# Kernel optimization log

Measured on AMD Instinct MI355X. Metric: run time of the kernel, lower is better.

Reference implementation:

```python
import jax, jax.numpy as jnp
import numpy as np

L = 6      # layers (enc and dec)
D = 512    # d_model
H = 8      # heads
DK = D // H
F = 2048   # dim_feedforward
B = 8
S = 512    # src len
T = 512    # tgt len
NEG = -1e9


def setup_inputs() -> dict:
    key = jax.random.key(0)
    ks = jax.random.split(key, 64)
    it = iter(ks)
    def w(shape, scale=0.02):
        return jax.random.normal(next(it), shape, dtype=jnp.float32) * scale
    inp = {}
    inp['src'] = jax.random.normal(next(it), (B, S, D), dtype=jnp.float32)
    inp['tgt'] = jax.random.normal(next(it), (B, T, D), dtype=jnp.float32)
    inp['tgt_mask'] = jnp.where(jnp.triu(jnp.ones((T, T), bool), 1), jnp.float32(NEG), jnp.float32(0.0))
    # encoder params (stacked over L layers)
    inp['enc_Wq'] = w((L, H, D, DK)); inp['enc_Wk'] = w((L, H, D, DK)); inp['enc_Wv'] = w((L, H, D, DK))
    inp['enc_Wo'] = w((L, D, D))
    inp['enc_ln1_a'] = jnp.ones((L, D)); inp['enc_ln1_b'] = jnp.zeros((L, D))
    inp['enc_W1'] = w((L, D, F)); inp['enc_b1'] = jnp.zeros((L, F))
    inp['enc_W2'] = w((L, F, D)); inp['enc_b2'] = jnp.zeros((L, D))
    inp['enc_ln2_a'] = jnp.ones((L, D)); inp['enc_ln2_b'] = jnp.zeros((L, D))
    # decoder params
    inp['dec_sWq'] = w((L, H, D, DK)); inp['dec_sWk'] = w((L, H, D, DK)); inp['dec_sWv'] = w((L, H, D, DK))
    inp['dec_sWo'] = w((L, D, D))
    inp['dec_ln1_a'] = jnp.ones((L, D)); inp['dec_ln1_b'] = jnp.zeros((L, D))
    inp['dec_cWq'] = w((L, H, D, DK)); inp['dec_cWk'] = w((L, H, D, DK)); inp['dec_cWv'] = w((L, H, D, DK))
    inp['dec_cWo'] = w((L, D, D))
    inp['dec_ln2_a'] = jnp.ones((L, D)); inp['dec_ln2_b'] = jnp.zeros((L, D))
    inp['dec_W1'] = w((L, D, F)); inp['dec_b1'] = jnp.zeros((L, F))
    inp['dec_W2'] = w((L, F, D)); inp['dec_b2'] = jnp.zeros((L, D))
    inp['dec_ln3_a'] = jnp.ones((L, D)); inp['dec_ln3_b'] = jnp.zeros((L, D))
    return inp


def layernorm(x, a, b):
    # faithful to the torch module: unbiased std (ddof=1) and eps added to std
    mean = x.mean(-1, keepdims=True)
    std = jnp.std(x, axis=-1, keepdims=True, ddof=1)
    return a * (x - mean) / (std + 1e-6) + b


def mha(qx, kx, vx, Wq, Wk, Wv, Wo, mask):
    # Wq/Wk/Wv: [H, D, dk] (per-head torch loop fused into one batched einsum)
    q = jnp.einsum('bsd,hdk->bhsk', qx, Wq)
    k = jnp.einsum('bsd,hdk->bhsk', kx, Wk)
    v = jnp.einsum('bsd,hdk->bhsk', vx, Wv)
    scores = jnp.einsum('bhqk,bhmk->bhqm', q, k) / np.float32(np.sqrt(Wq.shape[-1]))
    if mask is not None:
        scores = scores + mask  # [T,T] broadcasts over batch and heads
    attn = jax.nn.softmax(scores, axis=-1)
    o = jnp.einsum('bhqm,bhmk->bhqk', attn, v)
    b_, h_, s_, k_ = o.shape
    o = o.transpose(0, 2, 1, 3).reshape(b_, s_, h_ * k_)  # concat heads
    return o @ Wo


def ffn(x, W1, b1, W2, b2):
    return jnp.maximum(x @ W1 + b1, 0.0) @ W2 + b2


def reference(src, tgt, tgt_mask,
              enc_Wq, enc_Wk, enc_Wv, enc_Wo, enc_ln1_a, enc_ln1_b,
              enc_W1, enc_b1, enc_W2, enc_b2, enc_ln2_a, enc_ln2_b,
              dec_sWq, dec_sWk, dec_sWv, dec_sWo, dec_ln1_a, dec_ln1_b,
              dec_cWq, dec_cWk, dec_cWv, dec_cWo, dec_ln2_a, dec_ln2_b,
              dec_W1, dec_b1, dec_W2, dec_b2, dec_ln3_a, dec_ln3_b):
    # encoder
    x = src
    for i in range(L):
        h = x + mha(x, x, x, enc_Wq[i], enc_Wk[i], enc_Wv[i], enc_Wo[i], None)
        x = layernorm(h, enc_ln1_a[i], enc_ln1_b[i])
        h = x + ffn(x, enc_W1[i], enc_b1[i], enc_W2[i], enc_b2[i])
        x = layernorm(h, enc_ln2_a[i], enc_ln2_b[i])
    memory = x
    # decoder
    y = tgt
    for i in range(L):
        h = y + mha(y, y, y, dec_sWq[i], dec_sWk[i], dec_sWv[i], dec_sWo[i], tgt_mask)
        y = layernorm(h, dec_ln1_a[i], dec_ln1_b[i])
        h = y + mha(y, memory, memory, dec_cWq[i], dec_cWk[i], dec_cWv[i], dec_cWo[i], None)
        y = layernorm(h, dec_ln2_a[i], dec_ln2_b[i])
        h = y + ffn(y, dec_W1[i], dec_b1[i], dec_W2[i], dec_b2[i])
        y = layernorm(h, dec_ln3_a[i], dec_ln3_b[i])
    return y
```

## Files before the change

kernel.cpp:

```cpp
#include <hip/hip_runtime.h>
#include <hip/hip_bf16.h>

typedef unsigned short u16;
typedef __hip_bfloat16 hbf;
typedef __bf16 bf16x8 __attribute__((ext_vector_type(8)));
typedef float f32x4 __attribute__((ext_vector_type(4)));

#define LL 6
#define DD 512
#define HH 8
#define DKK 64
#define FF 2048
#define BB 8
#define SS 512

__global__ __launch_bounds__(256) void cvt_k(const float* __restrict__ x,
                                             hbf* __restrict__ y, int n) {
  for (int i = (blockIdx.x * 256 + threadIdx.x) * 4; i < n; i += gridDim.x * 1024) {
    float4 v = *(const float4*)(x + i);
    y[i] = __float2bfloat16(v.x);
    y[i + 1] = __float2bfloat16(v.y);
    y[i + 2] = __float2bfloat16(v.z);
    y[i + 3] = __float2bfloat16(v.w);
  }
}

__global__ __launch_bounds__(256) void transpose_k(const float* __restrict__ src,
                                                   hbf* __restrict__ dst, int R, int C) {
  __shared__ hbf tile[64][65];
  const int b = blockIdx.z;
  src += (size_t)b * R * C;
  dst += (size_t)b * R * C;
  int c0 = blockIdx.x * 64, r0 = blockIdx.y * 64;
  int tx = threadIdx.x & 63;
  int ty = threadIdx.x >> 6;
#pragma unroll
  for (int i = 0; i < 16; i++) {
    int r = ty + i * 4;
    tile[r][tx] = __float2bfloat16(src[(size_t)(r0 + r) * C + c0 + tx]);
  }
  __syncthreads();
#pragma unroll
  for (int i = 0; i < 16; i++) {
    int r = ty + i * 4;
    dst[(size_t)(c0 + r) * R + r0 + tx] = tile[tx][r];
  }
}

__global__ __launch_bounds__(256) void transpose_qkv_k(const float* __restrict__ Wq,
                                                       const float* __restrict__ Wk,
                                                       const float* __restrict__ Wv,
                                                       hbf* __restrict__ dst) {
  __shared__ hbf tile[64][65];
  const int z = blockIdx.z;
  const int l = z / 24, r = z - l * 24;
  const int zw = r >> 3, h = r & 7;
  const float* src =
      (zw == 0 ? Wq : (zw == 1 ? Wk : Wv)) + ((size_t)l * HH + h) * DD * DKK;
  const int r0 = blockIdx.y * 64;
  const int tx = threadIdx.x & 63, ty = threadIdx.x >> 6;
#pragma unroll
  for (int i = 0; i < 16; i++) {
    int rr = ty + i * 4;
    tile[rr][tx] = __float2bfloat16(src[(size_t)(r0 + rr) * DKK + tx]);
  }
  __syncthreads();
  hbf* d = dst + (size_t)l * 3 * DD * DD + ((size_t)zw * 512 + h * 64) * DD + r0;
#pragma unroll
  for (int i = 0; i < 16; i++) {
    int rr = ty + i * 4;
    d[(size_t)rr * DD + tx] = tile[tx][rr];
  }
}

template <int BM, int BN, int BK, int MODE, int SPLITK>
__global__ __launch_bounds__(256) void gemm_nt(
    const u16* __restrict__ A, const u16* __restrict__ Bm, void* __restrict__ Cout,
    void* __restrict__ C2, void* __restrict__ C3,
    const float* __restrict__ bias, const hbf* __restrict__ res,
    int M, int N, int K, int lda, int ldb, int ldc, int ncoloff,
    long sAo, long sAi, long sBo, long sBi, long sCo, long sCi, int inner, float scale) {
  constexpr int WVM = (BM == 128 && BN == 128) ? 2 : (BM == 128 ? 4 : 2);
  constexpr int WVN = 4 / WVM;
  constexpr int WTM = BM / WVM, WTN = BN / WVN;
  constexpr int AM = WTM / 16, AN = WTN / 16;
  constexpr int PA = (BM * BK) / 2048, PB = (BN * BK) / 2048;
  constexpr int CPR = BK / 8;
  __shared__ u16 As[BM][BK + 8];
  __shared__ u16 Bs[BN][BK + 8];

  int g = blockIdx.z;
  int ks = 0;
  if (SPLITK > 1) {
    ks = g;
    g = 0;
  }
  int outer = g / inner, inr = g - outer * inner;
  A += outer * sAo + inr * sAi;
  Bm += outer * sBo + inr * sBi;

  const int tid = threadIdx.x;
  const int m0 = blockIdx.y * BM, n0 = (blockIdx.x + ncoloff) * BN;
  const int wave = tid >> 6, lane = tid & 63;
  const int wm = (wave / WVN) * WTM, wn = (wave % WVN) * WTN;
  const int m16 = lane & 15, quad = lane >> 4;

  const u16* Ab = A + (size_t)m0 * lda;
  const u16* Bb = Bm + (size_t)n0 * ldb;

  f32x4 acc[AM][AN] = {};

  const int kbeg = ks * (K / SPLITK), kend = kbeg + K / SPLITK;
  for (int k0 = kbeg; k0 < kend; k0 += BK) {
#pragma unroll
    for (int p = 0; p < PA; p++) {
      int idx = p * 256 + tid;
      int row = idx / CPR, ch = (idx % CPR) * 8;
      *(float4*)(&As[row][ch]) = *(const float4*)(Ab + (size_t)row * lda + k0 + ch);
    }
#pragma unroll
    for (int p = 0; p < PB; p++) {
      int idx = p * 256 + tid;
      int row = idx / CPR, ch = (idx % CPR) * 8;
      *(float4*)(&Bs[row][ch]) = *(const float4*)(Bb + (size_t)row * ldb + k0 + ch);
    }
    __syncthreads();
#pragma unroll
    for (int kc = 0; kc < BK / 32; kc++) {
      bf16x8 af[AM], bfv[AN];
#pragma unroll
      for (int i = 0; i < AM; i++)
        af[i] = *(const bf16x8*)(&As[wm + i * 16 + m16][kc * 32 + quad * 8]);
#pragma unroll
      for (int j = 0; j < AN; j++)
        bfv[j] = *(const bf16x8*)(&Bs[wn + j * 16 + m16][kc * 32 + quad * 8]);
#pragma unroll
      for (int i = 0; i < AM; i++)
#pragma unroll
        for (int j = 0; j < AN; j++)
          acc[i][j] = __builtin_amdgcn_mfma_f32_16x16x32_bf16(af[i], bfv[j], acc[i][j], 0, 0, 0);
    }
    __syncthreads();
  }

#pragma unroll
  for (int i = 0; i < AM; i++) {
#pragma unroll
    for (int j = 0; j < AN; j++) {
      const int col = n0 + wn + j * 16 + m16;
      const int rowb = m0 + wm + i * 16 + quad * 4;
#pragma unroll
      for (int r = 0; r < 4; r++) {
        const int row = rowb + r;
        float v = acc[i][j][r] * scale;
        if (MODE == 0) {
          hbf* C = (hbf*)Cout + outer * sCo + inr * sCi;
          C[(size_t)row * ldc + col] = __float2bfloat16(v);
        } else if (MODE == 2) {
          float* C = (float*)((SPLITK > 1 && ks == 1) ? C2 : Cout);
          C += outer * sCo + inr * sCi;
          if (SPLITK == 1 || ks == 0) {
            if (bias) v += bias[col];
            if (res) v += __bfloat162float(res[(size_t)row * ldc + col]);
          }
          C[(size_t)row * ldc + col] = v;
        } else if (MODE == 3) {
          hbf* C = (hbf*)Cout + outer * sCo + inr * sCi;
          v += bias[col];
          C[(size_t)row * ldc + col] = __float2bfloat16(fmaxf(v, 0.0f));
        } else if (MODE == 4) {
          const int b = row >> 9, s = row & 511;
          const int which = col >> 9, h = (col >> 6) & 7, dk = col & 63;
          const int bh = (b << 3) + h;
          if (which == 0)
            ((hbf*)Cout)[((size_t)bh * SS + s) * DKK + dk] = __float2bfloat16(v * 0.125f);
          else if (which == 1)
            ((hbf*)C2)[((size_t)bh * SS + s) * DKK + dk] = __float2bfloat16(v);
          else
            ((hbf*)C3)[((size_t)bh * DKK + dk) * SS + s] = __float2bfloat16(v);
        }
      }
    }
  }
}

__global__ __launch_bounds__(256) void softmax_k(hbf* __restrict__ P, int causal) {
  const int row = blockIdx.x;
  hbf* p = P + ((size_t)blockIdx.y * SS + row) * SS;
  const int t = threadIdx.x;
  const int c0 = 2 * t, c1 = 2 * t + 1;
  float v0 = __bfloat162float(p[c0]);
  float v1 = __bfloat162float(p[c1]);
  if (causal) {
    if (c0 > row) v0 = -1e30f;
    if (c1 > row) v1 = -1e30f;
  }
  float m = fmaxf(v0, v1);
#pragma unroll
  for (int off = 32; off > 0; off >>= 1) m = fmaxf(m, __shfl_down(m, off));
  __shared__ float sm[4];
  __shared__ float bc;
  const int wv = t >> 6, ln = t & 63;
  if (ln == 0) sm[wv] = m;
  __syncthreads();
  if (t == 0) bc = fmaxf(fmaxf(sm[0], sm[1]), fmaxf(sm[2], sm[3]));
  __syncthreads();
  m = bc;
  float e0 = __expf(v0 - m), e1 = __expf(v1 - m);
  float s = e0 + e1;
#pragma unroll
  for (int off = 32; off > 0; off >>= 1) s += __shfl_down(s, off);
  __syncthreads();
  if (ln == 0) sm[wv] = s;
  __syncthreads();
  if (t == 0) bc = sm[0] + sm[1] + sm[2] + sm[3];
  __syncthreads();
  const float inv = 1.0f / bc;
  p[c0] = __float2bfloat16(e0 * inv);
  p[c1] = __float2bfloat16(e1 * inv);
}

template <typename T>
__global__ __launch_bounds__(256) void layernorm_k(const float* __restrict__ X,
                                                   const float* __restrict__ X2,
                                                   const float* __restrict__ ga,
                                                   const float* __restrict__ gb,
                                                   T* __restrict__ out, int Dn) {
  const int row = blockIdx.x;
  X += (size_t)row * Dn;
  X2 += (size_t)row * Dn;
  out += (size_t)row * Dn;
  const int t = threadIdx.x;
  float2 xv = *(const float2*)(X + 2 * t);
  float2 x2 = *(const float2*)(X2 + 2 * t);
  xv.x += x2.x;
  xv.y += x2.y;
  float s = xv.x + xv.y, ss = xv.x * xv.x + xv.y * xv.y;
#pragma unroll
  for (int off = 32; off > 0; off >>= 1) {
    s += __shfl_down(s, off);
    ss += __shfl_down(ss, off);
  }
  __shared__ float sm[8];
  __shared__ float smean, sinv;
  const int wv = t >> 6, ln = t & 63;
  if (ln == 0) {
    sm[wv] = s;
    sm[4 + wv] = ss;
  }
  __syncthreads();
  if (t == 0) {
    float S1 = sm[0] + sm[1] + sm[2] + sm[3];
    float S2 = sm[4] + sm[5] + sm[6] + sm[7];
    float mean = S1 / Dn;
    float var = (S2 - S1 * mean) / (Dn - 1);
    var = fmaxf(var, 0.0f);
    smean = mean;
    sinv = 1.0f / (sqrtf(var) + 1e-6f);
  }
  __syncthreads();
  const float mean = smean, inv = sinv;
  float o0 = ga[2 * t] * (xv.x - mean) * inv + gb[2 * t];
  float o1 = ga[2 * t + 1] * (xv.y - mean) * inv + gb[2 * t + 1];
  if constexpr (sizeof(T) == 2) {
    out[2 * t] = (T)__float2bfloat16(o0);
    out[2 * t + 1] = (T)__float2bfloat16(o1);
  } else {
    out[2 * t] = o0;
    out[2 * t + 1] = o1;
  }
}

extern "C" void kernel_launch(void* const* d_in, const int* in_sizes, int n_in,
                              void* d_out, int out_size, void* d_ws, size_t ws_size,
                              hipStream_t stream) {
  (void)in_sizes; (void)n_in; (void)out_size;
  const float* src = (const float*)d_in[0];
  const float* tgt = (const float*)d_in[1];
  const float* eWq = (const float*)d_in[3];
  const float* eWk = (const float*)d_in[4];
  const float* eWv = (const float*)d_in[5];
  const float* eWo = (const float*)d_in[6];
  const float* eln1a = (const float*)d_in[7];
  const float* eln1b = (const float*)d_in[8];
  const float* eW1 = (const float*)d_in[9];
  const float* eb1 = (const float*)d_in[10];
  const float* eW2 = (const float*)d_in[11];
  const float* eb2 = (const float*)d_in[12];
  const float* eln2a = (const float*)d_in[13];
  const float* eln2b = (const float*)d_in[14];
  const float* sWq = (const float*)d_in[15];
  const float* sWk = (const float*)d_in[16];
  const float* sWv = (const float*)d_in[17];
  const float* sWo = (const float*)d_in[18];
  const float* dln1a = (const float*)d_in[19];
  const float* dln1b = (const float*)d_in[20];
  const float* cWq = (const float*)d_in[21];
  const float* cWk = (const float*)d_in[22];
  const float* cWv = (const float*)d_in[23];
  const float* cWo = (const float*)d_in[24];
  const float* dln2a = (const float*)d_in[25];
  const float* dln2b = (const float*)d_in[26];
  const float* dW1 = (const float*)d_in[27];
  const float* db1 = (const float*)d_in[28];
  const float* dW2 = (const float*)d_in[29];
  const float* db2 = (const float*)d_in[30];
  const float* dln3a = (const float*)d_in[31];
  const float* dln3b = (const float*)d_in[32];

  const size_t MB = 1024 * 1024;
  char* ws = (char*)d_ws;
  const size_t QKV_L = (size_t)3 * DD * DD;
  const size_t WO_L = (size_t)DD * DD;
  const size_t WF_L = (size_t)DD * FF;
  const bool preT = ws_size >= 145 * MB;

  hbf *qkvT_all = nullptr, *woT_all = nullptr, *w1T_all = nullptr, *w2T_all = nullptr;
  hbf *wqkvS = nullptr, *woS = nullptr, *w1S = nullptr, *w2S = nullptr;
  char* actb;
  if (preT) {
    qkvT_all = (hbf*)(ws);
    woT_all = (hbf*)(ws + 28311552);
    w1T_all = (hbf*)(ws + 37748736);
    w2T_all = (hbf*)(ws + 62914560);
    actb = ws + 84 * MB;
  } else {
    if (ws_size < 67 * MB) return;
    wqkvS = (hbf*)(ws);
    woS = (hbf*)(ws + 2 * MB);
    w1S = (hbf*)(ws + 2 * MB + 512 * 1024);
    w2S = (hbf*)(ws + 4 * MB + 512 * 1024);
    actb = ws + 7 * MB;
  }
  hbf* sbuf = (hbf*)(actb);
  u16* xbuf = (u16*)(actb + 4 * MB);
  hbf* tbuf = (hbf*)(actb + 8 * MB);
  u16* ybuf = (u16*)(actb + 12 * MB);
  u16* qbuf = (u16*)(actb + 16 * MB);
  u16* kbuf = (u16*)(actb + 20 * MB);
  u16* vtb = (u16*)(actb + 24 * MB);
  u16* attnb = (u16*)(actb + 28 * MB);
  float* projf = (float*)(actb + 28 * MB);
  u16* ffnh = (u16*)(actb + 36 * MB);
  float* projf2 = (float*)(actb + 52 * MB);

  const long SD = (long)SS * DD;
  const long SDK = (long)SS * DKK;
  const long DKS = (long)DKK * SS;
  const long SSq = (long)SS * SS;
  const size_t WQL = (size_t)HH * DD * DKK;
  const size_t WOL = (size_t)DD * DD;
  const size_t WFL = (size_t)DD * FF;

  if (preT) {
    transpose_qkv_k<<<dim3(1, 8, LL * 24), dim3(256), 0, stream>>>(eWq, eWk, eWv, qkvT_all);
    transpose_qkv_k<<<dim3(1, 8, LL * 24), dim3(256), 0, stream>>>(sWq, sWk, sWv,
                                                                   qkvT_all + LL * QKV_L);
    transpose_qkv_k<<<dim3(1, 8, LL * 24), dim3(256), 0, stream>>>(
        cWq, cWk, cWv, qkvT_all + 2 * LL * QKV_L);
    transpose_k<<<dim3(8, 8, LL), dim3(256), 0, stream>>>(eWo, woT_all, DD, DD);
    transpose_k<<<dim3(8, 8, LL), dim3(256), 0, stream>>>(sWo, woT_all + LL * WO_L, DD, DD);
    transpose_k<<<dim3(8, 8, LL), dim3(256), 0, stream>>>(cWo, woT_all + 2 * LL * WO_L, DD, DD);
    transpose_k<<<dim3(32, 8, LL), dim3(256), 0, stream>>>(eW1, w1T_all, DD, FF);
    transpose_k<<<dim3(32, 8, LL), dim3(256), 0, stream>>>(dW1, w1T_all + LL * WF_L, DD, FF);
    transpose_k<<<dim3(8, 32, LL), dim3(256), 0, stream>>>(eW2, w2T_all, FF, DD);
    transpose_k<<<dim3(8, 32, LL), dim3(256), 0, stream>>>(dW2, w2T_all + LL * WF_L, FF, DD);
  }

  auto attention = [&](const u16* qin, const u16* kvin, const hbf* qkvTl, const hbf* woTl,
                       const u16* resid, int causal) {
    if (qin == kvin) {
      gemm_nt<64, 64, 128, 4, 1><<<dim3(24, 64, 1), dim3(256), 0, stream>>>(
          qin, (const u16*)qkvTl, qbuf, kbuf, vtb, nullptr, nullptr, BB * SS, 3 * DD, DD,
          DD, DD, 0, 0, 0, 0, 0, 0, 0, 0, 1, 1.f);
    } else {
      gemm_nt<64, 64, 128, 4, 1><<<dim3(8, 64, 1), dim3(256), 0, stream>>>(
          qin, (const u16*)qkvTl, qbuf, kbuf, vtb, nullptr, nullptr, BB * SS, DD, DD,
          DD, DD, 0, 0, 0, 0, 0, 0, 0, 0, 1, 1.f);
      gemm_nt<64, 64, 128, 4, 1><<<dim3(16, 64, 1), dim3(256), 0, stream>>>(
          kvin, (const u16*)qkvTl, qbuf, kbuf, vtb, nullptr, nullptr, BB * SS, 3 * DD, DD,
          DD, DD, 0, 8, 0, 0, 0, 0, 0, 0, 1, 1.f);
    }
    gemm_nt<128, 128, 64, 0, 1><<<dim3(4, 4, BB * HH), dim3(256), 0, stream>>>(
        qbuf, kbuf, attnb, nullptr, nullptr, nullptr, nullptr, SS, SS, DKK,
        DKK, DKK, SS, 0, SDK, 0, SDK, 0, SSq, 0, 1, 1.f);
    softmax_k<<<dim3(SS, BB * HH), dim3(256), 0, stream>>>((hbf*)attnb, causal);
    gemm_nt<64, 64, 128, 0, 1><<<dim3(1, 8, BB * HH), dim3(256), 0, stream>>>(
        attnb, vtb, qbuf, nullptr, nullptr, nullptr, nullptr, SS, DKK, SS,
        SS, SS, DD, 0, HH * SSq, SSq, HH * DKS, DKS, SD, DKK, HH, 1.f);
    gemm_nt<64, 64, 128, 2, 2><<<dim3(8, 64, 2), dim3(256), 0, stream>>>(
        qbuf, (const u16*)woTl, projf, projf2, nullptr, nullptr, (const hbf*)resid,
        BB * SS, DD, DD, DD, DD, DD, 0, 0, 0, 0, 0, 0, 0, 1, 1.f);
  };

  auto ffn = [&](const u16* xin, const hbf* w1Tl, const float* b1l, const hbf* w2Tl,
                 const float* b2l) {
    gemm_nt<64, 64, 128, 3, 1><<<dim3(32, 64, 1), dim3(256), 0, stream>>>(
        xin, (const u16*)w1Tl, ffnh, nullptr, nullptr, b1l, nullptr, BB * SS, FF, DD,
        DD, DD, FF, 0, 0, 0, 0, 0, 0, 0, 1, 1.f);
    gemm_nt<64, 64, 128, 2, 2><<<dim3(8, 64, 2), dim3(256), 0, stream>>>(
        ffnh, (const u16*)w2Tl, projf, projf2, nullptr, b2l, (const hbf*)xin, BB * SS, DD,
        FF, FF, FF, DD, 0, 0, 0, 0, 0, 0, 0, 1, 1.f);
  };

  auto lnb = [&](const float* X, const float* a, const float* b, u16* out) {
    layernorm_k<hbf><<<dim3(BB * SS), dim3(256), 0, stream>>>(X, projf2, a, b, (hbf*)out, DD);
  };

  cvt_k<<<dim3(2048), dim3(256), 0, stream>>>(src, sbuf, BB * SS * DD);
  cvt_k<<<dim3(2048), dim3(256), 0, stream>>>(tgt, tbuf, BB * SS * DD);

  const u16* cur = (const u16*)sbuf;
  for (int l = 0; l < LL; l++) {
    const hbf *qkvTl, *woTl, *w1Tl, *w2Tl;
    if (preT) {
      qkvTl = qkvT_all + (size_t)l * QKV_L;
      woTl = woT_all + (size_t)l * WO_L;
      w1Tl = w1T_all + (size_t)l * WF_L;
      w2Tl = w2T_all + (size_t)l * WF_L;
    } else {
      transpose_qkv_k<<<dim3(1, 8, 24), dim3(256), 0, stream>>>(
          eWq + l * WQL, eWk + l * WQL, eWv + l * WQL, wqkvS);
      transpose_k<<<dim3(8, 8, 1), dim3(256), 0, stream>>>(eWo + l * WOL, woS, DD, DD);
      qkvTl = wqkvS;
      woTl = woS;
    }
    attention(cur, cur, qkvTl, woTl, cur, 0);
    lnb(projf, eln1a + l * DD, eln1b + l * DD, xbuf);
    if (!preT) {
      transpose_k<<<dim3(32, 8, 1), dim3(256), 0, stream>>>(eW1 + l * WFL, w1S, DD, FF);
      transpose_k<<<dim3(8, 32, 1), dim3(256), 0, stream>>>(eW2 + l * WFL, w2S, FF, DD);
      w1Tl = w1S;
      w2Tl = w2S;
    }
    ffn(xbuf, w1Tl, eb1 + l * FF, w2Tl, eb2 + l * DD);
    lnb(projf, eln2a + l * DD, eln2b + l * DD, xbuf);
    cur = xbuf;
  }
  const u16* mem = cur;
  const u16* yc = (const u16*)tbuf;
  for (int l = 0; l < LL; l++) {
    const hbf *sqkvTl, *swoTl, *cqkvTl, *cwoTl, *w1Tl, *w2Tl;
    if (preT) {
      sqkvTl = qkvT_all + ((size_t)LL + l) * QKV_L;
      swoTl = woT_all + ((size_t)LL + l) * WO_L;
      cqkvTl = qkvT_all + ((size_t)2 * LL + l) * QKV_L;
      cwoTl = woT_all + ((size_t)2 * LL + l) * WO_L;
      w1Tl = w1T_all + ((size_t)LL + l) * WF_L;
      w2Tl = w2T_all + ((size_t)LL + l) * WF_L;
    }
    if (!preT) {
      transpose_qkv_k<<<dim3(1, 8, 24), dim3(256), 0, stream>>>(
          sWq + l * WQL, sWk + l * WQL, sWv + l * WQL, wqkvS);
      transpose_k<<<dim3(8, 8, 1), dim3(256), 0, stream>>>(sWo + l * WOL, woS, DD, DD);
      sqkvTl = wqkvS;
      swoTl = woS;
    }
    attention(yc, yc, sqkvTl, swoTl, yc, 1);
    lnb(projf, dln1a + l * DD, dln1b + l * DD, ybuf);
    yc = ybuf;
    if (!preT) {
      transpose_qkv_k<<<dim3(1, 8, 24), dim3(256), 0, stream>>>(
          cWq + l * WQL, cWk + l * WQL, cWv + l * WQL, wqkvS);
      transpose_k<<<dim3(8, 8, 1), dim3(256), 0, stream>>>(cWo + l * WOL, woS, DD, DD);
      cqkvTl = wqkvS;
      cwoTl = woS;
    }
    attention(yc, mem, cqkvTl, cwoTl, yc, 0);
    lnb(projf, dln2a + l * DD, dln2b + l * DD, ybuf);
    if (!preT) {
      transpose_k<<<dim3(32, 8, 1), dim3(256), 0, stream>>>(dW1 + l * WFL, w1S, DD, FF);
      transpose_k<<<dim3(8, 32, 1), dim3(256), 0, stream>>>(dW2 + l * WFL, w2S, FF, DD);
      w1Tl = w1S;
      w2Tl = w2S;
    }
    ffn(ybuf, w1Tl, db1 + l * FF, w2Tl, db2 + l * DD);
    if (l == LL - 1) {
      layernorm_k<float><<<dim3(BB * SS), dim3(256), 0, stream>>>(
          projf, projf2, dln3a + l * DD, dln3b + l * DD, (float*)d_out, DD);
    } else {
      lnb(projf, dln3a + l * DD, dln3b + l * DD, ybuf);
      yc = ybuf;
    }
  }
}
```

Measured before the change: 2.627 ms.

## Fuse QK^T, softmax and PV into a single attention kernel

```diff
diff --git a/kernel.cpp b/kernel.cpp
--- a/kernel.cpp
+++ b/kernel.cpp
@@ -184,40 +184,122 @@
   }
 }
 
-__global__ __launch_bounds__(256) void softmax_k(hbf* __restrict__ P, int causal) {
-  const int row = blockIdx.x;
-  hbf* p = P + ((size_t)blockIdx.y * SS + row) * SS;
-  const int t = threadIdx.x;
-  const int c0 = 2 * t, c1 = 2 * t + 1;
-  float v0 = __bfloat162float(p[c0]);
-  float v1 = __bfloat162float(p[c1]);
-  if (causal) {
-    if (c0 > row) v0 = -1e30f;
-    if (c1 > row) v1 = -1e30f;
-  }
-  float m = fmaxf(v0, v1);
-#pragma unroll
-  for (int off = 32; off > 0; off >>= 1) m = fmaxf(m, __shfl_down(m, off));
-  __shared__ float sm[4];
-  __shared__ float bc;
-  const int wv = t >> 6, ln = t & 63;
-  if (ln == 0) sm[wv] = m;
+__global__ __launch_bounds__(256) void flash_k(const u16* __restrict__ Q,
+                                               const u16* __restrict__ Kb,
+                                               const u16* __restrict__ Vt,
+                                               hbf* __restrict__ O, int causal) {
+  __shared__ u16 Qs[32][72];
+  __shared__ u16 Ks[128 * 72];
+  __shared__ u16 Ss[32][520];
+  const int bh = blockIdx.y;
+  const int q0 = blockIdx.x * 32;
+  const int b = bh >> 3, h = bh & 7;
+  const int tid = threadIdx.x;
+  const int wave = tid >> 6, lane = tid & 63;
+  const int m16 = lane & 15, quad = lane >> 4;
+  const int rg = (wave >> 1) * 16;
+  const int chf = wave & 1;
+
+  const u16* Qp = Q + ((size_t)bh * SS + q0) * DKK;
+  const u16* Kp = Kb + (size_t)bh * SS * DKK;
+  const u16* Vp = Vt + (size_t)bh * DKK * SS;
+
+  {
+    int row = tid >> 3, ch = (tid & 7) << 3;
+    *(float4*)(&Qs[row][ch]) = *(const float4*)(Qp + (size_t)row * DKK + ch);
+  }
+
+  for (int kt = 0; kt < 4; kt++) {
+    if (kt > 0) __syncthreads();
+#pragma unroll
+    for (int p = 0; p < 4; p++) {
+      int idx = p * 256 + tid;
+      int row = idx >> 3, ch = (idx & 7) << 3;
+      *(float4*)(&Ks[row * 72 + ch]) =
+          *(const float4*)(Kp + (size_t)(kt * 128 + row) * DKK + ch);
+    }
+    __syncthreads();
+#pragma unroll
+    for (int ct = 0; ct < 4; ct++) {
+      f32x4 s{};
+#pragma unroll
+      for (int kc = 0; kc < 2; kc++) {
+        bf16x8 a = *(const bf16x8*)(&Qs[rg + m16][kc * 32 + quad * 8]);
+        bf16x8 bv =
+            *(const bf16x8*)(&Ks[(chf * 64 + ct * 16 + m16) * 72 + kc * 32 + quad * 8]);
+        s = __builtin_amdgcn_mfma_f32_16x16x32_bf16(a, bv, s, 0, 0, 0);
+      }
+      const int colb = kt * 128 + chf * 64 + ct * 16 + m16;
+#pragma unroll
+      for (int r = 0; r < 4; r++)
+        *((hbf*)&Ss[rg + quad * 4 + r][colb]) = __float2bfloat16(s[r]);
+    }
+  }
   __syncthreads();
-  if (t == 0) bc = fmaxf(fmaxf(sm[0], sm[1]), fmaxf(sm[2], sm[3]));
+
+#pragma unroll
+  for (int rr = 0; rr < 8; rr++) {
+    const int r = wave * 8 + rr;
+    const int gr = q0 + r;
+    float v[8];
+#pragma unroll
+    for (int i = 0; i < 8; i++) {
+      const int col = lane + i * 64;
+      v[i] = __bfloat162float(((const hbf*)Ss[r])[col]);
+      if (causal && col > gr) v[i] = -1e30f;
+    }
+    float m = v[0];
+#pragma unroll
+    for (int i = 1; i < 8; i++) m = fmaxf(m, v[i]);
+#pragma unroll
+    for (int off = 1; off < 64; off <<= 1) m = fmaxf(m, __shfl_xor(m, off));
+    float e[8], s = 0.f;
+#pragma unroll
+    for (int i = 0; i < 8; i++) {
+      e[i] = __expf(v[i] - m);
+      s += e[i];
+    }
+#pragma unroll
+    for (int off = 1; off < 64; off <<= 1) s += __shfl_xor(s, off);
+    const float inv = 1.0f / s;
+#pragma unroll
+    for (int i = 0; i < 8; i++)
+      ((hbf*)Ss[r])[lane + i * 64] = __float2bfloat16(e[i] * inv);
+  }
   __syncthreads();
-  m = bc;
-  float e0 = __expf(v0 - m), e1 = __expf(v1 - m);
-  float s = e0 + e1;
-#pragma unroll
-  for (int off = 32; off > 0; off >>= 1) s += __shfl_down(s, off);
-  __syncthreads();
-  if (ln == 0) sm[wv] = s;
-  __syncthreads();
-  if (t == 0) bc = sm[0] + sm[1] + sm[2] + sm[3];
-  __syncthreads();
-  const float inv = 1.0f / bc;
-  p[c0] = __float2bfloat16(e0 * inv);
-  p[c1] = __float2bfloat16(e1 * inv);
+
+  f32x4 o[2] = {};
+  u16* Vs = Ks;
+  for (int vt = 0; vt < 4; vt++) {
+    if (vt > 0) __syncthreads();
+#pragma unroll
+    for (int p = 0; p < 4; p++) {
+      int idx = p * 256 + tid;
+      int row = idx >> 4, ch = (idx & 15) << 3;
+      *(float4*)(&Vs[row * 136 + ch]) =
+          *(const float4*)(Vp + (size_t)row * SS + vt * 128 + ch);
+    }
+    __syncthreads();
+#pragma unroll
+    for (int kc = 0; kc < 4; kc++) {
+      bf16x8 a = *(const bf16x8*)(&Ss[rg + m16][vt * 128 + kc * 32 + quad * 8]);
+#pragma unroll
+      for (int dt = 0; dt < 2; dt++) {
+        bf16x8 bv =
+            *(const bf16x8*)(&Vs[(chf * 32 + dt * 16 + m16) * 136 + kc * 32 + quad * 8]);
+        o[dt] = __builtin_amdgcn_mfma_f32_16x16x32_bf16(a, bv, o[dt], 0, 0, 0);
+      }
+    }
+  }
+#pragma unroll
+  for (int dt = 0; dt < 2; dt++) {
+    const int d = h * 64 + chf * 32 + dt * 16 + m16;
+#pragma unroll
+    for (int r = 0; r < 4; r++) {
+      const int row = q0 + rg + quad * 4 + r;
+      O[(size_t)b * SS * DD + (size_t)row * DD + d] = __float2bfloat16(o[dt][r]);
+    }
+  }
 }
 
 template <typename T>
@@ -313,7 +395,7 @@
   const size_t QKV_L = (size_t)3 * DD * DD;
   const size_t WO_L = (size_t)DD * DD;
   const size_t WF_L = (size_t)DD * FF;
-  const bool preT = ws_size >= 145 * MB;
+  const bool preT = ws_size >= 150 * MB;
 
   hbf *qkvT_all = nullptr, *woT_all = nullptr, *w1T_all = nullptr, *w2T_all = nullptr;
   hbf *wqkvS = nullptr, *woS = nullptr, *w1S = nullptr, *w2S = nullptr;
@@ -325,7 +407,7 @@
     w2T_all = (hbf*)(ws + 62914560);
     actb = ws + 84 * MB;
   } else {
-    if (ws_size < 67 * MB) return;
+    if (ws_size < 72 * MB) return;
     wqkvS = (hbf*)(ws);
     woS = (hbf*)(ws + 2 * MB);
     w1S = (hbf*)(ws + 2 * MB + 512 * 1024);
@@ -339,15 +421,11 @@
   u16* qbuf = (u16*)(actb + 16 * MB);
   u16* kbuf = (u16*)(actb + 20 * MB);
   u16* vtb = (u16*)(actb + 24 * MB);
-  u16* attnb = (u16*)(actb + 28 * MB);
-  float* projf = (float*)(actb + 28 * MB);
-  u16* ffnh = (u16*)(actb + 36 * MB);
-  float* projf2 = (float*)(actb + 52 * MB);
-
-  const long SD = (long)SS * DD;
-  const long SDK = (long)SS * DKK;
-  const long DKS = (long)DKK * SS;
-  const long SSq = (long)SS * SS;
+  u16* obuf = (u16*)(actb + 28 * MB);
+  u16* ffnh = (u16*)(actb + 32 * MB);
+  float* projf = (float*)(actb + 48 * MB);
+  float* projf2 = (float*)(actb + 56 * MB);
+
   const size_t WQL = (size_t)HH * DD * DKK;
   const size_t WOL = (size_t)DD * DD;
   const size_t WFL = (size_t)DD * FF;
@@ -381,15 +459,9 @@
           kvin, (const u16*)qkvTl, qbuf, kbuf, vtb, nullptr, nullptr, BB * SS, 3 * DD, DD,
           DD, DD, 0, 8, 0, 0, 0, 0, 0, 0, 1, 1.f);
     }
-    gemm_nt<128, 128, 64, 0, 1><<<dim3(4, 4, BB * HH), dim3(256), 0, stream>>>(
-        qbuf, kbuf, attnb, nullptr, nullptr, nullptr, nullptr, SS, SS, DKK,
-        DKK, DKK, SS, 0, SDK, 0, SDK, 0, SSq, 0, 1, 1.f);
-    softmax_k<<<dim3(SS, BB * HH), dim3(256), 0, stream>>>((hbf*)attnb, causal);
-    gemm_nt<64, 64, 128, 0, 1><<<dim3(1, 8, BB * HH), dim3(256), 0, stream>>>(
-        attnb, vtb, qbuf, nullptr, nullptr, nullptr, nullptr, SS, DKK, SS,
-        SS, SS, DD, 0, HH * SSq, SSq, HH * DKS, DKS, SD, DKK, HH, 1.f);
+    flash_k<<<dim3(16, 64), dim3(256), 0, stream>>>(qbuf, kbuf, vtb, (hbf*)obuf, causal);
     gemm_nt<64, 64, 128, 2, 2><<<dim3(8, 64, 2), dim3(256), 0, stream>>>(
-        qbuf, (const u16*)woTl, projf, projf2, nullptr, nullptr, (const hbf*)resid,
+        obuf, (const u16*)woTl, projf, projf2, nullptr, nullptr, (const hbf*)resid,
         BB * SS, DD, DD, DD, DD, DD, 0, 0, 0, 0, 0, 0, 0, 1, 1.f);
   };
 
```

Result: faster. 2.170 ms (-17.4%).
